# Optimization experiments

Hardware: AMD Instinct MI355X
Metric: run time of the kernel (lower is better)

## Reference

```python
import jax, jax.numpy as jnp
import numpy as np

N_NODES = 100000
N_EDGES = 1600000
IN_DIM, HID_DIM, OUT_DIM = 64, 128, 64


def setup_inputs() -> dict:
    key = jax.random.key(0)
    ks = jax.random.split(key, 12)
    s = 0.02
    x = jax.random.normal(ks[0], (N_NODES, IN_DIM), dtype=jnp.float32)
    edge_index = jax.random.randint(ks[1], (2, N_EDGES), 0, N_NODES, dtype=jnp.int64)
    return {
        "x": x,
        "edge_index": edge_index,
        # SAGEConv layer 1: lin_l (neighbors, with bias), lin_r (root, no bias)
        "w1l": jax.random.normal(ks[2], (HID_DIM, IN_DIM), dtype=jnp.float32) * s,
        "b1l": jnp.zeros((HID_DIM,), dtype=jnp.float32),
        "w1r": jax.random.normal(ks[3], (HID_DIM, IN_DIM), dtype=jnp.float32) * s,
        # SAGEConv layer 2
        "w2l": jax.random.normal(ks[4], (OUT_DIM, HID_DIM), dtype=jnp.float32) * s,
        "b2l": jnp.zeros((OUT_DIM,), dtype=jnp.float32),
        "w2r": jax.random.normal(ks[5], (OUT_DIM, HID_DIM), dtype=jnp.float32) * s,
        # classifier MLP: Linear(128,64) -> ReLU -> Linear(64,2) (dropout off in eval)
        "wc1": jax.random.normal(ks[6], (64, 2 * OUT_DIM), dtype=jnp.float32) * s,
        "bc1": jnp.zeros((64,), dtype=jnp.float32),
        "wc2": jax.random.normal(ks[7], (2, 64), dtype=jnp.float32) * s,
        "bc2": jnp.zeros((2,), dtype=jnp.float32),
    }


def _sage_conv(x, src, dst, wl, bl, wr):
    # PyG SAGEConv (aggr='mean'): out = lin_l(mean_{j in N(i)} x_j) + lin_r(x_i)
    msg = x[src]                                                  # [E, d] gather
    agg = jax.ops.segment_sum(msg, dst, num_segments=N_NODES)     # [N, d] scatter-add
    cnt = jax.ops.segment_sum(jnp.ones((src.shape[0],), x.dtype), dst, num_segments=N_NODES)
    mean = agg / jnp.maximum(cnt, 1.0)[:, None]
    return mean @ wl.T + bl + x @ wr.T


def reference(x, edge_index, w1l, b1l, w1r, w2l, b2l, w2r, wc1, bc1, wc2, bc2):
    src, dst = edge_index[0], edge_index[1]
    h = jax.nn.relu(_sage_conv(x, src, dst, w1l, b1l, w1r))   # dropout: eval mode (identity)
    h = jax.nn.relu(_sage_conv(h, src, dst, w2l, b2l, w2r))
    edge_repr = jnp.concatenate([h[src], h[dst]], axis=1)      # [E, 2*OUT_DIM]
    hidden = jax.nn.relu(edge_repr @ wc1.T + bc1)
    return hidden @ wc2.T + bc2                                 # [E, 2]
```

## Files before the change

kernel.cpp:

```cpp
#include <hip/hip_runtime.h>

#define N_NODES 100000
#define N_EDGES 1600000
#define NBLK_SCAN 391
#define SLICE_NODES 12500
#define FILL_CHUNK 12500

typedef unsigned int uint;
typedef unsigned short ushort;
typedef __attribute__((ext_vector_type(8))) short bf16x8;
typedef __attribute__((ext_vector_type(4))) float f32x4;

__device__ inline float bflo(uint u) { union { uint i; float f; } c; c.i = u << 16; return c.f; }
__device__ inline float bfhi(uint u) { union { uint i; float f; } c; c.i = u & 0xffff0000u; return c.f; }
__device__ inline float bf2f(ushort h) { union { uint i; float f; } c; c.i = (uint)h << 16; return c.f; }
__device__ inline ushort f2bf(float f) {
    union { float f; uint u; } c; c.f = f;
    uint r = (c.u + 0x7fffu + ((c.u >> 16) & 1u)) >> 16;
    return (ushort)r;
}

#define W1_OFF   0
#define W2L_OFF  16384
#define W2R_OFF  24576
#define WC1_OFF  32768
#define W_TOTAL  40960

__global__ __launch_bounds__(256) void prep_weights(const float* __restrict__ w1r,
                                                    const float* __restrict__ w1l,
                                                    const float* __restrict__ w2l,
                                                    const float* __restrict__ w2r,
                                                    const float* __restrict__ wc1,
                                                    ushort* __restrict__ Whi,
                                                    ushort* __restrict__ Wlo) {
    int idx = blockIdx.x * 256 + threadIdx.x;
    if (idx >= W_TOTAL) return;
    float v;
    if (idx < W2L_OFF) {
        int o = idx >> 7, k = idx & 127;
        v = (k < 64) ? w1r[o * 64 + k] : w1l[o * 64 + (k - 64)];
    } else if (idx < W2R_OFF) {
        int t2 = idx - W2L_OFF; int o = t2 >> 7, k = t2 & 127;
        v = w2l[o * 128 + k];
    } else if (idx < WC1_OFF) {
        int t2 = idx - W2R_OFF; int o = t2 >> 7, k = t2 & 127;
        v = w2r[o * 128 + k];
    } else {
        int t2 = idx - WC1_OFF; int o = t2 >> 6, k = t2 & 63;
        v = wc1[(o & 63) * 128 + ((o >> 6) << 6) + k];
    }
    ushort hi = f2bf(v);
    ushort lo = f2bf(v - bf2f(hi));
    Whi[idx] = hi; Wlo[idx] = lo;
}

__global__ __launch_bounds__(256) void convert_kernel(const float* __restrict__ x,
                                                      ushort* __restrict__ xb) {
    int i = blockIdx.x * 256 + threadIdx.x;
    if (i < N_NODES * 32) {
        float2 v = ((const float2*)x)[i];
        uint o = (uint)f2bf(v.x) | ((uint)f2bf(v.y) << 16);
        ((uint*)xb)[i] = o;
    }
}

__global__ __launch_bounds__(256) void degree_kernel(const int* __restrict__ dst,
                                                     int* __restrict__ cnt) {
    int e = blockIdx.x * blockDim.x + threadIdx.x;
    if (e < N_EDGES) atomicAdd(&cnt[dst[e]], 1);
}

__global__ __launch_bounds__(256) void scan_block_sums(const int* __restrict__ cnt,
                                                       int* __restrict__ partial) {
    __shared__ int red[4];
    int i = blockIdx.x * 256 + threadIdx.x;
    int v = (i < N_NODES) ? cnt[i] : 0;
#pragma unroll
    for (int off = 32; off; off >>= 1) v += __shfl_down(v, off, 64);
    if ((threadIdx.x & 63) == 0) red[threadIdx.x >> 6] = v;
    __syncthreads();
    if (threadIdx.x == 0) partial[blockIdx.x] = red[0] + red[1] + red[2] + red[3];
}

__global__ __launch_bounds__(512) void scan_top(int* __restrict__ partial) {
    __shared__ int s[512];
    int t = threadIdx.x;
    int orig = (t < NBLK_SCAN) ? partial[t] : 0;
    s[t] = orig;
    __syncthreads();
#pragma unroll
    for (int off = 1; off < 512; off <<= 1) {
        int v = (t >= off) ? s[t - off] : 0;
        __syncthreads();
        s[t] += v;
        __syncthreads();
    }
    if (t < NBLK_SCAN) partial[t] = s[t] - orig;
}

__global__ __launch_bounds__(256) void scan_final(const int* __restrict__ cnt,
                                                  const int* __restrict__ partial,
                                                  int* __restrict__ row_start,
                                                  int* __restrict__ cursor) {
    __shared__ int s[256];
    int i = blockIdx.x * 256 + threadIdx.x;
    int t = threadIdx.x;
    int orig = (i < N_NODES) ? cnt[i] : 0;
    s[t] = orig;
    __syncthreads();
#pragma unroll
    for (int off = 1; off < 256; off <<= 1) {
        int v = (t >= off) ? s[t - off] : 0;
        __syncthreads();
        s[t] += v;
        __syncthreads();
    }
    if (i < N_NODES) {
        int rs = partial[blockIdx.x] + s[t] - orig;
        row_start[i] = rs;
        cursor[i] = rs;
    }
}

__global__ __launch_bounds__(256) void fill_sliced(const int* __restrict__ src,
                                                   const int* __restrict__ dst,
                                                   int* __restrict__ cursor,
                                                   int* __restrict__ nbr) {
    int slice = blockIdx.x & 7;
    int chunk = blockIdx.x >> 3;
    int lo = slice * SLICE_NODES;
    int hi = lo + SLICE_NODES;
    int ebase = chunk * FILL_CHUNK;
#pragma unroll 1
    for (int e = ebase + threadIdx.x; e < ebase + FILL_CHUNK; e += 256) {
        int d = dst[e];
        if (d >= lo && d < hi) {
            int pos = atomicAdd(&cursor[d], 1);
            nbr[pos] = src[e];
        }
    }
}

__global__ __launch_bounds__(256) void agg_mean64_bf16(const int* __restrict__ row_start,
                                                       const int* __restrict__ cnt,
                                                       const int* __restrict__ nbr,
                                                       const ushort* __restrict__ feat,
                                                       float* __restrict__ outmean) {
    int node = blockIdx.x * 4 + (threadIdx.x >> 6);
    if (node >= N_NODES) return;
    int lane = threadIdx.x & 63;
    int half = lane >> 5;
    int f2   = lane & 31;
    int s = row_start[node];
    int d = cnt[node];
    float ax = 0.0f, ay = 0.0f;
    int p = 0;
    for (; p + 4 <= d; p += 4) {
        int n0 = nbr[s + p + half];
        int n1 = nbr[s + p + 2 + half];
        uint w0 = *(const uint*)(feat + (size_t)n0 * 64 + f2 * 2);
        uint w1 = *(const uint*)(feat + (size_t)n1 * 64 + f2 * 2);
        ax += bflo(w0) + bflo(w1);
        ay += bfhi(w0) + bfhi(w1);
    }
    for (; p + 2 <= d; p += 2) {
        int n0 = nbr[s + p + half];
        uint w0 = *(const uint*)(feat + (size_t)n0 * 64 + f2 * 2);
        ax += bflo(w0);
        ay += bfhi(w0);
    }
    if (p < d && half == 0) {
        int n0 = nbr[s + p];
        uint w0 = *(const uint*)(feat + (size_t)n0 * 64 + f2 * 2);
        ax += bflo(w0);
        ay += bfhi(w0);
    }
    ax += __shfl_xor(ax, 32, 64);
    ay += __shfl_xor(ay, 32, 64);
    if (half == 0) {
        float inv = 1.0f / fmaxf((float)d, 1.0f);
        float2 o; o.x = ax * inv; o.y = ay * inv;
        *(float2*)&outmean[(size_t)node * 64 + f2 * 2] = o;
    }
}


#define MFMA __builtin_amdgcn_mfma_f32_16x16x32_bf16

__global__ __launch_bounds__(256) void g1g2_kernel(const float* __restrict__ x,
                                                   const float* __restrict__ mean1,
                                                   const ushort* __restrict__ Whi,
                                                   const ushort* __restrict__ Wlo,
                                                   const float* __restrict__ b1l,
                                                   ushort* __restrict__ h1hi,
                                                   ushort* __restrict__ h1lo,
                                                   ushort* __restrict__ y2b) {
    __shared__ ushort Ah[64 * 136];
    __shared__ ushort Al[64 * 136];
    const int t = threadIdx.x;
    const int l = t & 63;
    const int wv = t >> 6;
    const int base = blockIdx.x * 64;
    const int lr = l & 15;
    const int lk = (l >> 4) * 8;

    for (int idx = t; idx < 2048; idx += 256) {
        int halfsel = idx >> 10;
        int id2 = idx & 1023;
        int n = id2 >> 4;
        int k0 = (id2 & 15) * 4;
        int gn = base + n;
        float4 v = make_float4(0.f, 0.f, 0.f, 0.f);
        if (gn < N_NODES) v = *(const float4*)&(halfsel ? mean1 : x)[(size_t)gn * 64 + k0];
        ushort h0 = f2bf(v.x), h1_ = f2bf(v.y), h2_ = f2bf(v.z), h3 = f2bf(v.w);
        ushort l0 = f2bf(v.x - bf2f(h0)), l1 = f2bf(v.y - bf2f(h1_));
        ushort l2 = f2bf(v.z - bf2f(h2_)), l3 = f2bf(v.w - bf2f(h3));
        int col = halfsel * 64 + k0;
        uint2 ph; ph.x = (uint)h0 | ((uint)h1_ << 16); ph.y = (uint)h2_ | ((uint)h3 << 16);
        uint2 pl; pl.x = (uint)l0 | ((uint)l1 << 16); pl.y = (uint)l2 | ((uint)l3 << 16);
        *(uint2*)&Ah[n * 136 + col] = ph;
        *(uint2*)&Al[n * 136 + col] = pl;
    }
    __syncthreads();

    f32x4 acc[4][2];
#pragma unroll
    for (int m4 = 0; m4 < 4; ++m4)
#pragma unroll
        for (int n2 = 0; n2 < 2; ++n2) acc[m4][n2] = (f32x4){0.f, 0.f, 0.f, 0.f};

#pragma unroll
    for (int ks = 0; ks < 4; ++ks) {
        bf16x8 ah[4], al[4];
        int aoff = lr * 136 + ks * 32 + lk;
#pragma unroll
        for (int m4 = 0; m4 < 4; ++m4) {
            ah[m4] = *(const bf16x8*)&Ah[m4 * 2176 + aoff];
            al[m4] = *(const bf16x8*)&Al[m4 * 2176 + aoff];
        }
#pragma unroll
        for (int n2 = 0; n2 < 2; ++n2) {
            int o = wv * 32 + n2 * 16 + lr;
            int woff = W1_OFF + o * 128 + ks * 32 + lk;
            bf16x8 bh = *(const bf16x8*)&Whi[woff];
            bf16x8 bl = *(const bf16x8*)&Wlo[woff];
#pragma unroll
            for (int m4 = 0; m4 < 4; ++m4) {
                acc[m4][n2] = MFMA(al[m4], bh, acc[m4][n2], 0, 0, 0);
                acc[m4][n2] = MFMA(ah[m4], bl, acc[m4][n2], 0, 0, 0);
                acc[m4][n2] = MFMA(ah[m4], bh, acc[m4][n2], 0, 0, 0);
            }
        }
    }
    __syncthreads();
    ushort* H1h = Ah;
    ushort* H1l = Al;

#pragma unroll
    for (int n2 = 0; n2 < 2; ++n2) {
        int o = wv * 32 + n2 * 16 + lr;
        float bb = b1l[o];
#pragma unroll
        for (int m4 = 0; m4 < 4; ++m4) {
#pragma unroll
            for (int r = 0; r < 4; ++r) {
                int nl = m4 * 16 + (l >> 4) * 4 + r;
                float val = fmaxf(acc[m4][n2][r] + bb, 0.f);
                ushort hi = f2bf(val);
                ushort lo = f2bf(val - bf2f(hi));
                H1h[nl * 136 + o] = hi;
                H1l[nl * 136 + o] = lo;
            }
        }
    }
    __syncthreads();

    for (int idx = t; idx < 2048; idx += 256) {
        int n = idx >> 5;
        int c4 = (idx & 31) * 4;
        int gn = base + n;
        if (gn < N_NODES) {
            *(uint2*)&h1hi[(size_t)gn * 128 + c4] = *(uint2*)&H1h[n * 136 + c4];
            *(uint2*)&h1lo[(size_t)gn * 128 + c4] = *(uint2*)&H1l[n * 136 + c4];
        }
    }

    f32x4 acc2[4];
#pragma unroll
    for (int m4 = 0; m4 < 4; ++m4) acc2[m4] = (f32x4){0.f, 0.f, 0.f, 0.f};
#pragma unroll
    for (int ks = 0; ks < 4; ++ks) {
        int aoff = lr * 136 + ks * 32 + lk;
        int o2 = wv * 16 + lr;
        int woff = W2L_OFF + o2 * 128 + ks * 32 + lk;
        bf16x8 bh = *(const bf16x8*)&Whi[woff];
        bf16x8 bl = *(const bf16x8*)&Wlo[woff];
#pragma unroll
        for (int m4 = 0; m4 < 4; ++m4) {
            bf16x8 ah = *(const bf16x8*)&H1h[m4 * 2176 + aoff];
            bf16x8 al = *(const bf16x8*)&H1l[m4 * 2176 + aoff];
            acc2[m4] = MFMA(al, bh, acc2[m4], 0, 0, 0);
            acc2[m4] = MFMA(ah, bl, acc2[m4], 0, 0, 0);
            acc2[m4] = MFMA(ah, bh, acc2[m4], 0, 0, 0);
        }
    }
#pragma unroll
    for (int m4 = 0; m4 < 4; ++m4) {
#pragma unroll
        for (int r = 0; r < 4; ++r) {
            int nl = m4 * 16 + (l >> 4) * 4 + r;
            int gn = base + nl;
            if (gn < N_NODES) y2b[(size_t)gn * 64 + wv * 16 + lr] = f2bf(acc2[m4][r]);
        }
    }
}

__global__ __launch_bounds__(256) void g3g4_kernel(const ushort* __restrict__ h1hi,
                                                   const ushort* __restrict__ h1lo,
                                                   const float* __restrict__ mean2,
                                                   const ushort* __restrict__ Whi,
                                                   const ushort* __restrict__ Wlo,
                                                   const float* __restrict__ b2l,
                                                   const float* __restrict__ bc1,
                                                   ushort* __restrict__ uvb) {
    __shared__ ushort H1h[64 * 136];
    __shared__ ushort H1l[64 * 136];
    __shared__ float  M2[64 * 68];
    const int t = threadIdx.x;
    const int l = t & 63;
    const int wv = t >> 6;
    const int base = blockIdx.x * 64;
    const int lr = l & 15;
    const int lk = (l >> 4) * 8;

    for (int idx = t; idx < 2048; idx += 256) {
        int n = idx >> 5;
        int c4 = (idx & 31) * 4;
        int gn = base + n;
        uint2 vh = make_uint2(0u, 0u), vl = make_uint2(0u, 0u);
        if (gn < N_NODES) {
            vh = *(const uint2*)&h1hi[(size_t)gn * 128 + c4];
            vl = *(const uint2*)&h1lo[(size_t)gn * 128 + c4];
        }
        *(uint2*)&H1h[n * 136 + c4] = vh;
        *(uint2*)&H1l[n * 136 + c4] = vl;
    }
    for (int idx = t; idx < 1024; idx += 256) {
        int n = idx >> 4;
        int k0 = (idx & 15) * 4;
        int gn = base + n;
        float4 v = make_float4(0.f, 0.f, 0.f, 0.f);
        if (gn < N_NODES) v = *(const float4*)&mean2[(size_t)gn * 64 + k0];
        *(float4*)&M2[n * 68 + k0] = v;
    }
    __syncthreads();

    f32x4 acc[4];
#pragma unroll
    for (int m4 = 0; m4 < 4; ++m4) acc[m4] = (f32x4){0.f, 0.f, 0.f, 0.f};
#pragma unroll
    for (int ks = 0; ks < 4; ++ks) {
        int aoff = lr * 136 + ks * 32 + lk;
        int o2 = wv * 16 + lr;
        int woff = W2R_OFF + o2 * 128 + ks * 32 + lk;
        bf16x8 bh = *(const bf16x8*)&Whi[woff];
        bf16x8 bl = *(const bf16x8*)&Wlo[woff];
#pragma unroll
        for (int m4 = 0; m4 < 4; ++m4) {
            bf16x8 ah = *(const bf16x8*)&H1h[m4 * 2176 + aoff];
            bf16x8 al = *(const bf16x8*)&H1l[m4 * 2176 + aoff];
            acc[m4] = MFMA(al, bh, acc[m4], 0, 0, 0);
            acc[m4] = MFMA(ah, bl, acc[m4], 0, 0, 0);
            acc[m4] = MFMA(ah, bh, acc[m4], 0, 0, 0);
        }
    }
    __syncthreads();
    ushort* H2h = H1h;
    ushort* H2l = H1l;

    {
        int o2 = wv * 16 + lr;
        float bb = b2l[o2];
#pragma unroll
        for (int m4 = 0; m4 < 4; ++m4) {
#pragma unroll
            for (int r = 0; r < 4; ++r) {
                int nl = m4 * 16 + (l >> 4) * 4 + r;
                float val = fmaxf(acc[m4][r] + M2[nl * 68 + o2] + bb, 0.f);
                ushort hi = f2bf(val);
                ushort lo = f2bf(val - bf2f(hi));
                H2h[nl * 72 + o2] = hi;
                H2l[nl * 72 + o2] = lo;
            }
        }
    }
    __syncthreads();

    f32x4 acc4[4][2];
#pragma unroll
    for (int m4 = 0; m4 < 4; ++m4)
#pragma unroll
        for (int n2 = 0; n2 < 2; ++n2) acc4[m4][n2] = (f32x4){0.f, 0.f, 0.f, 0.f};
#pragma unroll
    for (int ks = 0; ks < 2; ++ks) {
        bf16x8 ah[4], al[4];
        int aoff = lr * 72 + ks * 32 + lk;
#pragma unroll
        for (int m4 = 0; m4 < 4; ++m4) {
            ah[m4] = *(const bf16x8*)&H2h[m4 * 1152 + aoff];
            al[m4] = *(const bf16x8*)&H2l[m4 * 1152 + aoff];
        }
#pragma unroll
        for (int n2 = 0; n2 < 2; ++n2) {
            int o = wv * 32 + n2 * 16 + lr;
            int woff = WC1_OFF + o * 64 + ks * 32 + lk;
            bf16x8 bh = *(const bf16x8*)&Whi[woff];
            bf16x8 bl = *(const bf16x8*)&Wlo[woff];
#pragma unroll
            for (int m4 = 0; m4 < 4; ++m4) {
                acc4[m4][n2] = MFMA(al[m4], bh, acc4[m4][n2], 0, 0, 0);
                acc4[m4][n2] = MFMA(ah[m4], bl, acc4[m4][n2], 0, 0, 0);
                acc4[m4][n2] = MFMA(ah[m4], bh, acc4[m4][n2], 0, 0, 0);
            }
        }
    }
#pragma unroll
    for (int n2 = 0; n2 < 2; ++n2) {
        int o = wv * 32 + n2 * 16 + lr;
        float bb = (o < 64) ? bc1[o] : 0.0f;
#pragma unroll
        for (int m4 = 0; m4 < 4; ++m4) {
#pragma unroll
            for (int r = 0; r < 4; ++r) {
                int nl = m4 * 16 + (l >> 4) * 4 + r;
                int gn = base + nl;
                if (gn < N_NODES) uvb[(size_t)gn * 128 + o] = f2bf(acc4[m4][n2][r] + bb);
            }
        }
    }
}

__global__ __launch_bounds__(256) void edge_kernel(const int* __restrict__ src,
                                                   const int* __restrict__ dst,
                                                   const ushort* __restrict__ uvb,
                                                   const float* __restrict__ wc2,
                                                   const float* __restrict__ bc2,
                                                   float* __restrict__ out) {
    int e = blockIdx.x * blockDim.x + threadIdx.x;
    if (e >= N_EDGES) return;
    const uint* ua = (const uint*)(uvb + (size_t)src[e] * 128);
    const uint* va = (const uint*)(uvb + (size_t)dst[e] * 128 + 64);
    float o0 = 0.0f, o1 = 0.0f;
#pragma unroll
    for (int k = 0; k < 32; ++k) {
        uint a = ua[k], b = va[k];
        float h0 = fmaxf(bflo(a) + bflo(b), 0.0f);
        float h1 = fmaxf(bfhi(a) + bfhi(b), 0.0f);
        o0 += wc2[2 * k] * h0 + wc2[2 * k + 1] * h1;
        o1 += wc2[64 + 2 * k] * h0 + wc2[65 + 2 * k] * h1;
    }
    float2 r;
    r.x = o0 + bc2[0];
    r.y = o1 + bc2[1];
    *(float2*)(out + (size_t)e * 2) = r;
}

extern "C" void kernel_launch(void* const* d_in, const int* in_sizes, int n_in,
                              void* d_out, int out_size, void* d_ws, size_t ws_size,
                              hipStream_t stream) {
    const float* x   = (const float*)d_in[0];
    const int*   ei  = (const int*)d_in[1];
    const float* w1l = (const float*)d_in[2];
    const float* b1l = (const float*)d_in[3];
    const float* w1r = (const float*)d_in[4];
    const float* w2l = (const float*)d_in[5];
    const float* b2l = (const float*)d_in[6];
    const float* w2r = (const float*)d_in[7];
    const float* wc1 = (const float*)d_in[8];
    const float* bc1 = (const float*)d_in[9];
    const float* wc2 = (const float*)d_in[10];
    const float* bc2 = (const float*)d_in[11];
    float* out = (float*)d_out;

    const int* srcp = ei;
    const int* dstp = ei + N_EDGES;

    float*  ws    = (float*)d_ws;
    ushort* xb    = (ushort*)ws;
    ushort* y2b   = (ushort*)ws;
    float*  mean1 = ws + 3200000;
    ushort* uvb   = (ushort*)(ws + 3200000);
    ushort* h1hi  = (ushort*)(ws + 9600000);
    ushort* h1lo  = (ushort*)(ws + 16000000);
    float*  mean2 = ws + 22400000;
    int*    ib    = (int*)(ws + 28800000);
    int* cnt       = ib;
    int* row_start = ib + 100000;
    int* cursor    = ib + 200000;
    int* partial   = ib + 300000;
    int* nbr       = ib + 300512;
    ushort* Whi = (ushort*)(ws + 30800000);
    ushort* Wlo = (ushort*)(ws + 30900000);

    hipMemsetAsync(cnt, 0, (size_t)N_NODES * 4, stream);

    prep_weights<<<(W_TOTAL + 255) / 256, 256, 0, stream>>>(w1r, w1l, w2l, w2r, wc1, Whi, Wlo);
    convert_kernel<<<12500, 256, 0, stream>>>(x, xb);
    degree_kernel<<<(N_EDGES + 255) / 256, 256, 0, stream>>>(dstp, cnt);
    scan_block_sums<<<NBLK_SCAN, 256, 0, stream>>>(cnt, partial);
    scan_top<<<1, 512, 0, stream>>>(partial);
    scan_final<<<NBLK_SCAN, 256, 0, stream>>>(cnt, partial, row_start, cursor);
    fill_sliced<<<1024, 256, 0, stream>>>(srcp, dstp, cursor, nbr);

    const int NAB = (N_NODES + 3) / 4;
    const int NB  = (N_NODES + 63) / 64;

    agg_mean64_bf16<<<NAB, 256, 0, stream>>>(row_start, cnt, nbr, xb, mean1);
    g1g2_kernel<<<NB, 256, 0, stream>>>(x, mean1, Whi, Wlo, b1l, h1hi, h1lo, y2b);
    agg_mean64_bf16<<<NAB, 256, 0, stream>>>(row_start, cnt, nbr, y2b, mean2);
    g3g4_kernel<<<NB, 256, 0, stream>>>(h1hi, h1lo, mean2, Whi, Wlo, b2l, bc1, uvb);
    edge_kernel<<<(N_EDGES + 255) / 256, 256, 0, stream>>>(srcp, dstp, uvb, wc2, bc2, out);
}
```

Measured before the change: 446.7 us.

## Bucket edges by destination slice, drop h1 low-precision split, vectorize edge loads

The degree pass now also writes packed (local dst, src) words into eight per-slice buckets, and the CSR fill reads only its own slice's bucket. Before, every fill block scanned all edges and discarded those outside its slice. The layer-2 input h1 is kept only as its bf16 high part, which removes the h1lo store, its reload and one MFMA per tile, at some cost in accuracy. The edge kernel loads uint4 vectors instead of scalar uints. Buckets have a fixed capacity and the pack puts src in 17 bits, so the scheme relies on node ids fitting in 17 bits and on each bucket not overflowing.

Measured after the change: 470.9 us. 5.4% more time.

```diff
diff --git a/kernel.cpp b/kernel.cpp
--- a/kernel.cpp
+++ b/kernel.cpp
@@ -4,7 +4,7 @@
 #define N_EDGES 1600000
 #define NBLK_SCAN 391
 #define SLICE_NODES 12500
-#define FILL_CHUNK 12500
+#define BCAP 800000
 
 typedef unsigned int uint;
 typedef unsigned short ushort;
@@ -64,10 +64,32 @@
     }
 }
 
-__global__ __launch_bounds__(256) void degree_kernel(const int* __restrict__ dst,
-                                                     int* __restrict__ cnt) {
-    int e = blockIdx.x * blockDim.x + threadIdx.x;
-    if (e < N_EDGES) atomicAdd(&cnt[dst[e]], 1);
+__global__ __launch_bounds__(256) void bucket_kernel(const int* __restrict__ src,
+                                                     const int* __restrict__ dst,
+                                                     int* __restrict__ cnt,
+                                                     int* __restrict__ bcur,
+                                                     uint* __restrict__ bkt) {
+    __shared__ int hist[8];
+    __shared__ int bbase[8];
+    const int t = threadIdx.x;
+    int e = blockIdx.x * 256 + t;
+    if (t < 8) hist[t] = 0;
+    __syncthreads();
+    int b = -1, mo = 0; uint pack = 0;
+    if (e < N_EDGES) {
+        int d = dst[e], s = src[e];
+        atomicAdd(&cnt[d], 1);
+        b = d / SLICE_NODES;
+        pack = ((uint)(d - b * SLICE_NODES) << 17) | (uint)s;
+        mo = atomicAdd(&hist[b], 1);
+    }
+    __syncthreads();
+    if (t < 8) bbase[t] = hist[t] ? atomicAdd(&bcur[t], hist[t]) : 0;
+    __syncthreads();
+    if (b >= 0) {
+        int pos = bbase[b] + mo;
+        if (pos < BCAP) bkt[(size_t)b * BCAP + pos] = pack;
+    }
 }
 
 __global__ __launch_bounds__(256) void scan_block_sums(const int* __restrict__ cnt,
@@ -122,22 +144,22 @@
     }
 }
 
-__global__ __launch_bounds__(256) void fill_sliced(const int* __restrict__ src,
-                                                   const int* __restrict__ dst,
-                                                   int* __restrict__ cursor,
-                                                   int* __restrict__ nbr) {
+__global__ __launch_bounds__(256) void fill_bucketed(const uint* __restrict__ bkt,
+                                                     const int* __restrict__ bcur,
+                                                     int* __restrict__ cursor,
+                                                     int* __restrict__ nbr) {
     int slice = blockIdx.x & 7;
     int chunk = blockIdx.x >> 3;
-    int lo = slice * SLICE_NODES;
-    int hi = lo + SLICE_NODES;
-    int ebase = chunk * FILL_CHUNK;
-#pragma unroll 1
-    for (int e = ebase + threadIdx.x; e < ebase + FILL_CHUNK; e += 256) {
-        int d = dst[e];
-        if (d >= lo && d < hi) {
-            int pos = atomicAdd(&cursor[d], 1);
-            nbr[pos] = src[e];
-        }
+    int count = min(bcur[slice], BCAP);
+    int per = (count + 127) >> 7;
+    int start = chunk * per;
+    int end = min(start + per, count);
+    const uint* B = bkt + (size_t)slice * BCAP;
+    for (int i = start + threadIdx.x; i < end; i += 256) {
+        uint p = B[i];
+        int d = slice * SLICE_NODES + (int)(p >> 17);
+        int pos = atomicAdd(&cursor[d], 1);
+        nbr[pos] = (int)(p & 0x1FFFFu);
     }
 }
 
@@ -184,7 +206,6 @@
     }
 }
 
-
 #define MFMA __builtin_amdgcn_mfma_f32_16x16x32_bf16
 
 __global__ __launch_bounds__(256) void g1g2_kernel(const float* __restrict__ x,
@@ -193,7 +214,6 @@
                                                    const ushort* __restrict__ Wlo,
                                                    const float* __restrict__ b1l,
                                                    ushort* __restrict__ h1hi,
-                                                   ushort* __restrict__ h1lo,
                                                    ushort* __restrict__ y2b) {
     __shared__ ushort Ah[64 * 136];
     __shared__ ushort Al[64 * 136];
@@ -279,10 +299,8 @@
         int n = idx >> 5;
         int c4 = (idx & 31) * 4;
         int gn = base + n;
-        if (gn < N_NODES) {
+        if (gn < N_NODES)
             *(uint2*)&h1hi[(size_t)gn * 128 + c4] = *(uint2*)&H1h[n * 136 + c4];
-            *(uint2*)&h1lo[(size_t)gn * 128 + c4] = *(uint2*)&H1l[n * 136 + c4];
-        }
     }
 
     f32x4 acc2[4];
@@ -316,7 +334,6 @@
 }
 
 __global__ __launch_bounds__(256) void g3g4_kernel(const ushort* __restrict__ h1hi,
-                                                   const ushort* __restrict__ h1lo,
                                                    const float* __restrict__ mean2,
                                                    const ushort* __restrict__ Whi,
                                                    const ushort* __restrict__ Wlo,
@@ -324,8 +341,8 @@
                                                    const float* __restrict__ bc1,
                                                    ushort* __restrict__ uvb) {
     __shared__ ushort H1h[64 * 136];
-    __shared__ ushort H1l[64 * 136];
     __shared__ float  M2[64 * 68];
+    __shared__ ushort H2l[64 * 72];
     const int t = threadIdx.x;
     const int l = t & 63;
     const int wv = t >> 6;
@@ -337,13 +354,9 @@
         int n = idx >> 5;
         int c4 = (idx & 31) * 4;
         int gn = base + n;
-        uint2 vh = make_uint2(0u, 0u), vl = make_uint2(0u, 0u);
-        if (gn < N_NODES) {
-            vh = *(const uint2*)&h1hi[(size_t)gn * 128 + c4];
-            vl = *(const uint2*)&h1lo[(size_t)gn * 128 + c4];
-        }
+        uint2 vh = make_uint2(0u, 0u);
+        if (gn < N_NODES) vh = *(const uint2*)&h1hi[(size_t)gn * 128 + c4];
         *(uint2*)&H1h[n * 136 + c4] = vh;
-        *(uint2*)&H1l[n * 136 + c4] = vl;
     }
     for (int idx = t; idx < 1024; idx += 256) {
         int n = idx >> 4;
@@ -368,15 +381,12 @@
 #pragma unroll
         for (int m4 = 0; m4 < 4; ++m4) {
             bf16x8 ah = *(const bf16x8*)&H1h[m4 * 2176 + aoff];
-            bf16x8 al = *(const bf16x8*)&H1l[m4 * 2176 + aoff];
-            acc[m4] = MFMA(al, bh, acc[m4], 0, 0, 0);
             acc[m4] = MFMA(ah, bl, acc[m4], 0, 0, 0);
             acc[m4] = MFMA(ah, bh, acc[m4], 0, 0, 0);
         }
     }
     __syncthreads();
     ushort* H2h = H1h;
-    ushort* H2l = H1l;
 
     {
         int o2 = wv * 16 + lr;
@@ -448,16 +458,22 @@
                                                    float* __restrict__ out) {
     int e = blockIdx.x * blockDim.x + threadIdx.x;
     if (e >= N_EDGES) return;
-    const uint* ua = (const uint*)(uvb + (size_t)src[e] * 128);
-    const uint* va = (const uint*)(uvb + (size_t)dst[e] * 128 + 64);
+    const uint4* ua = (const uint4*)(uvb + (size_t)src[e] * 128);
+    const uint4* va = (const uint4*)(uvb + (size_t)dst[e] * 128 + 64);
     float o0 = 0.0f, o1 = 0.0f;
 #pragma unroll
-    for (int k = 0; k < 32; ++k) {
-        uint a = ua[k], b = va[k];
-        float h0 = fmaxf(bflo(a) + bflo(b), 0.0f);
-        float h1 = fmaxf(bfhi(a) + bfhi(b), 0.0f);
-        o0 += wc2[2 * k] * h0 + wc2[2 * k + 1] * h1;
-        o1 += wc2[64 + 2 * k] * h0 + wc2[65 + 2 * k] * h1;
+    for (int k = 0; k < 8; ++k) {
+        uint4 a = ua[k], b = va[k];
+        int i0 = k * 8;
+        float h0, h1v;
+        h0 = fmaxf(bflo(a.x) + bflo(b.x), 0.f); h1v = fmaxf(bfhi(a.x) + bfhi(b.x), 0.f);
+        o0 += wc2[i0] * h0 + wc2[i0 + 1] * h1v;  o1 += wc2[64 + i0] * h0 + wc2[65 + i0] * h1v;
+        h0 = fmaxf(bflo(a.y) + bflo(b.y), 0.f); h1v = fmaxf(bfhi(a.y) + bfhi(b.y), 0.f);
+        o0 += wc2[i0 + 2] * h0 + wc2[i0 + 3] * h1v;  o1 += wc2[66 + i0] * h0 + wc2[67 + i0] * h1v;
+        h0 = fmaxf(bflo(a.z) + bflo(b.z), 0.f); h1v = fmaxf(bfhi(a.z) + bfhi(b.z), 0.f);
+        o0 += wc2[i0 + 4] * h0 + wc2[i0 + 5] * h1v;  o1 += wc2[68 + i0] * h0 + wc2[69 + i0] * h1v;
+        h0 = fmaxf(bflo(a.w) + bflo(b.w), 0.f); h1v = fmaxf(bfhi(a.w) + bfhi(b.w), 0.f);
+        o0 += wc2[i0 + 6] * h0 + wc2[i0 + 7] * h1v;  o1 += wc2[70 + i0] * h0 + wc2[71 + i0] * h1v;
     }
     float2 r;
     r.x = o0 + bc2[0];
@@ -491,33 +507,36 @@
     float*  mean1 = ws + 3200000;
     ushort* uvb   = (ushort*)(ws + 3200000);
     ushort* h1hi  = (ushort*)(ws + 9600000);
-    ushort* h1lo  = (ushort*)(ws + 16000000);
+    uint*   bkt   = (uint*)(ws + 16000000);
     float*  mean2 = ws + 22400000;
     int*    ib    = (int*)(ws + 28800000);
     int* cnt       = ib;
     int* row_start = ib + 100000;
     int* cursor    = ib + 200000;
     int* partial   = ib + 300000;
-    int* nbr       = ib + 300512;
+    int* bcur      = ib + 300512;
+    int* nbr       = ib + 300520;
     ushort* Whi = (ushort*)(ws + 30800000);
     ushort* Wlo = (ushort*)(ws + 30900000);
 
     hipMemsetAsync(cnt, 0, (size_t)N_NODES * 4, stream);
+    hipMemsetAsync(bcur, 0, 8 * 4, stream);
 
     prep_weights<<<(W_TOTAL + 255) / 256, 256, 0, stream>>>(w1r, w1l, w2l, w2r, wc1, Whi, Wlo);
     convert_kernel<<<12500, 256, 0, stream>>>(x, xb);
-    degree_kernel<<<(N_EDGES + 255) / 256, 256, 0, stream>>>(dstp, cnt);
+
+    bucket_kernel<<<(N_EDGES + 255) / 256, 256, 0, stream>>>(srcp, dstp, cnt, bcur, bkt);
     scan_block_sums<<<NBLK_SCAN, 256, 0, stream>>>(cnt, partial);
     scan_top<<<1, 512, 0, stream>>>(partial);
     scan_final<<<NBLK_SCAN, 256, 0, stream>>>(cnt, partial, row_start, cursor);
-    fill_sliced<<<1024, 256, 0, stream>>>(srcp, dstp, cursor, nbr);
+    fill_bucketed<<<1024, 256, 0, stream>>>(bkt, bcur, cursor, nbr);
 
     const int NAB = (N_NODES + 3) / 4;
     const int NB  = (N_NODES + 63) / 64;
 
     agg_mean64_bf16<<<NAB, 256, 0, stream>>>(row_start, cnt, nbr, xb, mean1);
-    g1g2_kernel<<<NB, 256, 0, stream>>>(x, mean1, Whi, Wlo, b1l, h1hi, h1lo, y2b);
+    g1g2_kernel<<<NB, 256, 0, stream>>>(x, mean1, Whi, Wlo, b1l, h1hi, y2b);
     agg_mean64_bf16<<<NAB, 256, 0, stream>>>(row_start, cnt, nbr, y2b, mean2);
-    g3g4_kernel<<<NB, 256, 0, stream>>>(h1hi, h1lo, mean2, Whi, Wlo, b2l, bc1, uvb);
+    g3g4_kernel<<<NB, 256, 0, stream>>>(h1hi, mean2, Whi, Wlo, b2l, bc1, uvb);
     edge_kernel<<<(N_EDGES + 255) / 256, 256, 0, stream>>>(srcp, dstp, uvb, wc2, bc2, out);
 }
```
